# Performance work log

Hardware: AMD Instinct MI355X
Metric: run time of the kernel (lower is better)

The kernel has to match this reference:

```python
import jax, jax.numpy as jnp
import numpy as np

B, T, I, H = 512, 1024, 50, 32  # batch, seq_len, input_size, hidden_size


def setup_inputs() -> dict:
    key = jax.random.key(0)
    ks = jax.random.split(key, 13)
    s = 1.0 / np.sqrt(H)  # PyTorch LSTM/Linear uniform init bound

    def u(k, shape):
        return jax.random.uniform(k, shape, jnp.float32, -s, s)

    return {
        "x": jax.random.normal(ks[0], (B, T, I), jnp.float32),
        # forward direction LSTM params (gate order: i, f, g, o)
        "w_ih_f": u(ks[1], (4 * H, I)),
        "w_hh_f": u(ks[2], (4 * H, H)),
        "b_ih_f": u(ks[3], (4 * H,)),
        "b_hh_f": u(ks[4], (4 * H,)),
        # reverse direction LSTM params
        "w_ih_r": u(ks[5], (4 * H, I)),
        "w_hh_r": u(ks[6], (4 * H, H)),
        "b_ih_r": u(ks[7], (4 * H,)),
        "b_hh_r": u(ks[8], (4 * H,)),
        # FC head
        "fc1_w": u(ks[9], (2 * H, 2 * H)),
        "fc1_b": u(ks[10], (2 * H,)),
        "fc3_w": u(ks[11], (1, 2 * H)),
        "fc3_b": u(ks[12], (1,)),
    }


def _lstm_scan(x_proj, w_hh):
    # x_proj: (T, B, 4H) = precomputed input projections + biases
    b = x_proj.shape[1]
    h0 = jnp.zeros((b, H), x_proj.dtype)
    c0 = jnp.zeros((b, H), x_proj.dtype)

    def step(carry, xp):
        h, c = carry
        z = xp + h @ w_hh.T  # (B, 4H)
        i, f, g, o = jnp.split(z, 4, axis=-1)
        c = jax.nn.sigmoid(f) * c + jax.nn.sigmoid(i) * jnp.tanh(g)
        h = jax.nn.sigmoid(o) * jnp.tanh(c)
        return (h, c), h

    _, hs = jax.lax.scan(step, (h0, c0), x_proj)
    return hs  # (T, B, H)


def reference(x, w_ih_f, w_hh_f, b_ih_f, b_hh_f,
              w_ih_r, w_hh_r, b_ih_r, b_hh_r,
              fc1_w, fc1_b, fc3_w, fc3_b):
    xt = jnp.swapaxes(x, 0, 1)  # (T, B, I) time-major for scan
    # batch all input projections up front (big GEMM instead of per-step)
    pf = xt @ w_ih_f.T + (b_ih_f + b_hh_f)          # (T, B, 4H)
    pr = xt[::-1] @ w_ih_r.T + (b_ih_r + b_hh_r)    # reversed time

    hf = _lstm_scan(pf, w_hh_f)           # (T, B, H)
    hr = _lstm_scan(pr, w_hh_r)[::-1]     # flip back to forward time order

    out = jnp.concatenate([hf, hr], axis=-1)  # (T, B, 2H)
    out = jnp.swapaxes(out, 0, 1)             # (B, T, 2H)
    out = out @ fc1_w.T + fc1_b               # fc1
    # dropout(p=0.2) is identity in eval/inference mode
    out = out @ fc3_w.T + fc3_b               # fc3 -> (B, T, 1)
    return out
```

## Files before the change

### kernel.cpp

```cpp
#include <hip/hip_runtime.h>

#define BB 512
#define TT 1024
#define II 50
#define HH 32
#define CH 16
#define NCH (TT / CH)
#define RSLOT 32

typedef float v2f __attribute__((ext_vector_type(2)));
typedef float v4f __attribute__((ext_vector_type(4)));
typedef short v8s __attribute__((ext_vector_type(8)));

__device__ __forceinline__ float fast_rcp(float x) { return __builtin_amdgcn_rcpf(x); }
__device__ __forceinline__ float sigm(float x) { return fast_rcp(1.f + __expf(-x)); }
__device__ __forceinline__ float tanh_(float x) {
    return 1.f - 2.f * fast_rcp(1.f + __expf(2.f * x));
}
__device__ __forceinline__ short bf16rne(float f) {
    unsigned u = __float_as_uint(f);
    u += 0x7FFF + ((u >> 16) & 1);
    return (short)(u >> 16);
}

#if __has_builtin(__builtin_amdgcn_permlane32_swap)
typedef unsigned v2u __attribute__((ext_vector_type(2)));
__device__ __forceinline__ float xhalf_sum(float p) {
    v2u r = __builtin_amdgcn_permlane32_swap(__float_as_uint(p),
                                             __float_as_uint(p), false, false);
    return __uint_as_float(r.x) + __uint_as_float(r.y);
}
#else
__device__ __forceinline__ float xhalf_sum(float p) {
    return p + __shfl_xor(p, 32, 64);
}
#endif

__global__ void init_out_kernel(float* __restrict__ out,
                                const float* __restrict__ fc1_b,
                                const float* __restrict__ fc3_w,
                                const float* __restrict__ fc3_b,
                                int n) {
    int idx = blockIdx.x * blockDim.x + threadIdx.x;
    float b = fc3_b[0];
    #pragma unroll
    for (int k = 0; k < 64; ++k) b += fc3_w[k] * fc1_b[k];
    if (idx < n) out[idx] = b;
}

__global__ void __launch_bounds__(384, 1) lstm_pc_kernel(
    const float* __restrict__ x,
    const float* __restrict__ w_ih_f, const float* __restrict__ w_hh_f,
    const float* __restrict__ b_ih_f, const float* __restrict__ b_hh_f,
    const float* __restrict__ w_ih_r, const float* __restrict__ w_hh_r,
    const float* __restrict__ b_ih_r, const float* __restrict__ b_hh_r,
    const float* __restrict__ fc1_w, const float* __restrict__ fc3_w,
    float* __restrict__ out)
{
    __shared__ float ringF[2][RSLOT * 256];
    __shared__ float hbuf[2][2][HH][65];
    __shared__ __align__(16) float hst[2][64];

    const int tid  = threadIdx.x;
    const int lane = tid & 63;
    const int wave = tid >> 6;
    const int is_prod = (wave >= 4);
    const int sb   = is_prod ? (wave - 4) : (wave >> 1);
    const int b    = blockIdx.x * 2 + sb;
    float* outb = out + (size_t)b * TT;
    float* ring = ringF[sb];

    if (is_prod) {
        const float* xb = x + (size_t)b * TT * II;
        const int nl = lane & 15;
        const int q  = lane >> 4;
        const float* wih[2] = {w_ih_f, w_ih_r};

        v8s Bf[2][8][2];
        #pragma unroll
        for (int d = 0; d < 2; ++d)
            #pragma unroll
            for (int nt = 0; nt < 8; ++nt) {
                const int n = nt * 16 + nl;
                #pragma unroll
                for (int kf = 0; kf < 2; ++kf)
                    #pragma unroll
                    for (int j = 0; j < 8; ++j) {
                        const int k = kf * 32 + q * 8 + j;
                        Bf[d][nt][kf][j] = (k < II) ? bf16rne(wih[d][n * II + k])
                                                    : (short)0;
                    }
            }

        auto cidx = [](int g) -> int {
            return (g < 32) ? 2 * g
                 : (g < 64) ? 2 * (g - 32) + 1
                 : (g < 96) ? 64 + 2 * (g - 64)
                            : 64 + 2 * (g - 96) + 1;
        };

        auto produce_chunk = [&](int c) {
            #pragma unroll
            for (int d = 0; d < 2; ++d) {
                const int S = c * CH + nl;
                const int t = d ? (TT - 1 - S) : S;
                const float* xr = xb + (size_t)t * II;
                v8s A0, A1;
                #pragma unroll
                for (int j = 0; j < 8; ++j) A0[j] = bf16rne(xr[q * 8 + j]);
                #pragma unroll
                for (int j = 0; j < 8; ++j) {
                    const int k = 32 + q * 8 + j;
                    A1[j] = (k < II) ? bf16rne(xr[k]) : (short)0;
                }
                #pragma unroll
                for (int nt = 0; nt < 8; ++nt) {
                    v4f acc = {0.f, 0.f, 0.f, 0.f};
                    acc = __builtin_amdgcn_mfma_f32_16x16x32_bf16(A0, Bf[d][nt][0], acc, 0, 0, 0);
                    acc = __builtin_amdgcn_mfma_f32_16x16x32_bf16(A1, Bf[d][nt][1], acc, 0, 0, 0);
                    const int col = d * 128 + cidx(nt * 16 + nl);
                    #pragma unroll
                    for (int r = 0; r < 4; ++r) {
                        const int slot = (c * CH + q * 4 + r) & (RSLOT - 1);
                        ring[slot * 256 + col] = acc[r];
                    }
                }
            }
        };
        auto flush = [&](int m) {
            if (lane < 32) {
                const int d   = lane >> 4;
                const int idx = lane & 15;
                const int ti  = m * CH + idx;
                const int col = ti & 63;
                float d0 = 0.f, d1 = 0.f, d2 = 0.f, d3 = 0.f;
                #pragma unroll
                for (int k = 0; k < HH; k += 4) {
                    d0 += hbuf[sb][d][k    ][col];
                    d1 += hbuf[sb][d][k + 1][col];
                    d2 += hbuf[sb][d][k + 2][col];
                    d3 += hbuf[sb][d][k + 3][col];
                }
                const int t = d ? (TT - 1 - ti) : ti;
                atomicAdd(&outb[t], (d0 + d1) + (d2 + d3));
            }
        };

        produce_chunk(0);
        __syncthreads();
        for (int n = 0; n < NCH; ++n) {
            if (n + 1 < NCH) produce_chunk(n + 1);
            if (n >= 1) flush(n - 1);
            __syncthreads();
        }
        flush(NCH - 1);
    } else {
        const int d  = wave & 1;
        const int k  = lane & 31;
        const int kh = lane >> 5;
        const float* w_hh = d ? w_hh_r : w_hh_f;
        const float* bi   = d ? b_ih_r : b_ih_f;
        const float* bh   = d ? b_hh_r : b_hh_f;

        v2f wp[4][8];
        float bseed[4];
        #pragma unroll
        for (int D = 0; D < 4; ++D) {
            const int row = D * 32 + k;
            #pragma unroll
            for (int j = 0; j < 8; ++j) {
                wp[D][j].x = w_hh[row * HH + 16 * kh + 2 * j];
                wp[D][j].y = w_hh[row * HH + 16 * kh + 2 * j + 1];
            }
            bseed[D] = kh ? 0.f : (bi[row] + bh[row]);
        }

        float wc = 0.f;
        {
            const int j = d * HH + k;
            #pragma unroll
            for (int n = 0; n < 64; ++n) wc += fc3_w[n] * fc1_w[n * 64 + j];
        }

        hst[sb][d * 32 + k] = 0.f;
        float c = 0.f;

        __syncthreads();

        for (int n = 0; n < NCH; ++n) {
            const int slot0 = (n & 1) * CH;
            const int col0  = (n & 3) * CH;
            #pragma unroll
            for (int u = 0; u < CH; ++u) {
                const float* rp = &ring[(slot0 + u) * 256 + d * 128 + 2 * k];
                const v2f xz1 = *(const v2f*)rp;
                const v2f xz2 = *(const v2f*)(rp + 64);

                float4 h4[4];
                #pragma unroll
                for (int j = 0; j < 4; ++j)
                    h4[j] = *(const float4*)&hst[sb][d * 32 + kh * 16 + 4 * j];

                v2f acc[4];
                #pragma unroll
                for (int D = 0; D < 4; ++D) acc[D] = (v2f){bseed[D], 0.f};
                #pragma unroll
                for (int j = 0; j < 4; ++j) {
                    v2f p0 = {h4[j].x, h4[j].y};
                    v2f p1 = {h4[j].z, h4[j].w};
                    #pragma unroll
                    for (int D = 0; D < 4; ++D) {
                        acc[D] = __builtin_elementwise_fma(p0, wp[D][2 * j    ], acc[D]);
                        acc[D] = __builtin_elementwise_fma(p1, wp[D][2 * j + 1], acc[D]);
                    }
                }
                const float zi = xhalf_sum(acc[0].x + acc[0].y) + xz1.x;
                const float zf = xhalf_sum(acc[1].x + acc[1].y) + xz1.y;
                const float zg = xhalf_sum(acc[2].x + acc[2].y) + xz2.x;
                const float zo = xhalf_sum(acc[3].x + acc[3].y) + xz2.y;

                const float gi = sigm(zi);
                const float gf = sigm(zf);
                const float gg = tanh_(zg);
                const float go = sigm(zo);

                c = fmaf(gf, c, gi * gg);
                const float h = go * tanh_(c);

                hst[sb][d * 32 + k] = h;
                hbuf[sb][d][k][col0 + u] = h * wc;
                asm volatile("" ::: "memory");
            }
            __syncthreads();
        }
    }
}

extern "C" void kernel_launch(void* const* d_in, const int* in_sizes, int n_in,
                              void* d_out, int out_size, void* d_ws, size_t ws_size,
                              hipStream_t stream) {
    const float* x      = (const float*)d_in[0];
    const float* w_ih_f = (const float*)d_in[1];
    const float* w_hh_f = (const float*)d_in[2];
    const float* b_ih_f = (const float*)d_in[3];
    const float* b_hh_f = (const float*)d_in[4];
    const float* w_ih_r = (const float*)d_in[5];
    const float* w_hh_r = (const float*)d_in[6];
    const float* b_ih_r = (const float*)d_in[7];
    const float* b_hh_r = (const float*)d_in[8];
    const float* fc1_w  = (const float*)d_in[9];
    const float* fc1_b  = (const float*)d_in[10];
    const float* fc3_w  = (const float*)d_in[11];
    const float* fc3_b  = (const float*)d_in[12];
    float* out = (float*)d_out;

    const int n = BB * TT;
    init_out_kernel<<<(n + 255) / 256, 256, 0, stream>>>(out, fc1_b, fc3_w, fc3_b, n);

    lstm_pc_kernel<<<BB / 2, 384, 0, stream>>>(
        x, w_ih_f, w_hh_f, b_ih_f, b_hh_f,
        w_ih_r, w_hh_r, b_ih_r, b_hh_r,
        fc1_w, fc3_w, out);
}
```

Measured before the change: 418.7 us.

## Split LSTM gates across half-waves and broadcast hidden state via readlane

The recurrent step is reorganized so each half-wave computes two full gate rows (i/f or g/o) over all 32 hidden inputs, rather than each lane computing partial sums of all four gates that must be reduced across halves. The hidden state is broadcast with readlane from registers instead of being written to and reread from LDS each step. Gate activations are exchanged between halves with a single cross-half swap, and tanh for g is computed through a scaled sigmoid. This targets LDS round-trip latency and reduction work on the serial critical path, at the cost of 32 scalar readlanes per step and more weight registers per lane.

After: 425.7 us. No clear change (+1.7%).

```diff
diff --git a/kernel.cpp b/kernel.cpp
--- a/kernel.cpp
+++ b/kernel.cpp
@@ -21,6 +21,9 @@
     unsigned u = __float_as_uint(f);
     u += 0x7FFF + ((u >> 16) & 1);
     return (short)(u >> 16);
+}
+__device__ __forceinline__ float rlane(float v, int l) {
+    return __int_as_float(__builtin_amdgcn_readlane(__float_as_int(v), l));
 }
 
 #if __has_builtin(__builtin_amdgcn_permlane32_swap)
@@ -59,7 +62,6 @@
 {
     __shared__ float ringF[2][RSLOT * 256];
     __shared__ float hbuf[2][2][HH][65];
-    __shared__ __align__(16) float hst[2][64];
 
     const int tid  = threadIdx.x;
     const int lane = tid & 63;
@@ -157,23 +159,25 @@
     } else {
         const int d  = wave & 1;
         const int k  = lane & 31;
-        const int kh = lane >> 5;
+        const int gh = lane >> 5;
         const float* w_hh = d ? w_hh_r : w_hh_f;
         const float* bi   = d ? b_ih_r : b_ih_f;
         const float* bh   = d ? b_hh_r : b_hh_f;
 
-        v2f wp[4][8];
-        float bseed[4];
+        const int rowA = gh ? (64 + k) : k;
+        const int rowB = gh ? (96 + k) : (32 + k);
+        v2f wpA[16], wpB[16];
         #pragma unroll
-        for (int D = 0; D < 4; ++D) {
-            const int row = D * 32 + k;
-            #pragma unroll
-            for (int j = 0; j < 8; ++j) {
-                wp[D][j].x = w_hh[row * HH + 16 * kh + 2 * j];
-                wp[D][j].y = w_hh[row * HH + 16 * kh + 2 * j + 1];
-            }
-            bseed[D] = kh ? 0.f : (bi[row] + bh[row]);
-        }
+        for (int j = 0; j < 16; ++j) {
+            wpA[j].x = w_hh[rowA * HH + 2 * j];
+            wpA[j].y = w_hh[rowA * HH + 2 * j + 1];
+            wpB[j].x = w_hh[rowB * HH + 2 * j];
+            wpB[j].y = w_hh[rowB * HH + 2 * j + 1];
+        }
+        const float bA = bi[rowA] + bh[rowA];
+        const float bB = bi[rowB] + bh[rowB];
+        const float mm = gh ? 2.f : 1.f;
+        const float aa = gh ? -1.f : 0.f;
 
         float wc = 0.f;
         {
@@ -182,8 +186,8 @@
             for (int n = 0; n < 64; ++n) wc += fc3_w[n] * fc1_w[n * 64 + j];
         }
 
-        hst[sb][d * 32 + k] = 0.f;
         float c = 0.f;
+        float h = 0.f;
 
         __syncthreads();
 
@@ -192,44 +196,39 @@
             const int col0  = (n & 3) * CH;
             #pragma unroll
             for (int u = 0; u < CH; ++u) {
-                const float* rp = &ring[(slot0 + u) * 256 + d * 128 + 2 * k];
-                const v2f xz1 = *(const v2f*)rp;
-                const v2f xz2 = *(const v2f*)(rp + 64);
-
-                float4 h4[4];
-                #pragma unroll
-                for (int j = 0; j < 4; ++j)
-                    h4[j] = *(const float4*)&hst[sb][d * 32 + kh * 16 + 4 * j];
-
-                v2f acc[4];
-                #pragma unroll
-                for (int D = 0; D < 4; ++D) acc[D] = (v2f){bseed[D], 0.f};
-                #pragma unroll
-                for (int j = 0; j < 4; ++j) {
-                    v2f p0 = {h4[j].x, h4[j].y};
-                    v2f p1 = {h4[j].z, h4[j].w};
-                    #pragma unroll
-                    for (int D = 0; D < 4; ++D) {
-                        acc[D] = __builtin_elementwise_fma(p0, wp[D][2 * j    ], acc[D]);
-                        acc[D] = __builtin_elementwise_fma(p1, wp[D][2 * j + 1], acc[D]);
-                    }
-                }
-                const float zi = xhalf_sum(acc[0].x + acc[0].y) + xz1.x;
-                const float zf = xhalf_sum(acc[1].x + acc[1].y) + xz1.y;
-                const float zg = xhalf_sum(acc[2].x + acc[2].y) + xz2.x;
-                const float zo = xhalf_sum(acc[3].x + acc[3].y) + xz2.y;
-
-                const float gi = sigm(zi);
-                const float gf = sigm(zf);
-                const float gg = tanh_(zg);
-                const float go = sigm(zo);
-
-                c = fmaf(gf, c, gi * gg);
-                const float h = go * tanh_(c);
-
-                hst[sb][d * 32 + k] = h;
+                const v2f xz = *(const v2f*)&ring[(slot0 + u) * 256 + d * 128
+                                                  + gh * 64 + 2 * k];
+
+                float hs[32];
+                #pragma unroll
+                for (int j = 0; j < 32; ++j) hs[j] = rlane(h, j);
+
+                v2f aA = (v2f){bA, 0.f};
+                v2f aB = (v2f){bB, 0.f};
+                #pragma unroll
+                for (int j = 0; j < 16; ++j) {
+                    const v2f hp = {hs[2 * j], hs[2 * j + 1]};
+                    aA = __builtin_elementwise_fma(hp, wpA[j], aA);
+                    aB = __builtin_elementwise_fma(hp, wpB[j], aB);
+                }
+                const float zA = xz.x + aA.x + aA.y;
+                const float zB = xz.y + aB.x + aB.y;
+
+                const float actA = fmaf(sigm(zA * mm), mm, aa);
+                const float actB = sigm(zB);
+
+                const float pA = xhalf_sum(actA) - actA;
+                const float pB = xhalf_sum(actB) - actB;
+
+                const float si = gh ? pA   : actA;
+                const float tg = gh ? actA : pA;
+                const float sf = gh ? pB   : actB;
+                const float so = gh ? actB : pB;
+
+                c = fmaf(sf, c, si * tg);
+                h = so * tanh_(c);
+
                 hbuf[sb][d][k][col0 + u] = h * wc;
-                asm volatile("" ::: "memory");
             }
             __syncthreads();
         }
```
